# Performance work log

Measured on AMD Instinct MI355X. Metric: run time of the kernel, lower is better.

## Reference

```python
import jax, jax.numpy as jnp
import numpy as np

D_MODEL = 1024
NUM_HEADS = 16
D_K = D_MODEL // NUM_HEADS
ROPE_BASE = 10000.0


def _rope_cos_sin(seq_len, d_k):
    inv_freq = 1.0 / (ROPE_BASE ** (jnp.arange(0, d_k, 2, dtype=jnp.float32) / d_k))
    t = jnp.arange(seq_len, dtype=jnp.float32)
    freqs = t[:, None] * inv_freq[None, :]          # [S, d_k/2]
    emb = jnp.concatenate([freqs, freqs], axis=-1)  # [S, d_k]
    return jnp.cos(emb), jnp.sin(emb)


def _rotate_half(x):
    x1, x2 = jnp.split(x, 2, axis=-1)
    return jnp.concatenate([-x2, x1], axis=-1)


def setup_inputs() -> dict:
    key = jax.random.key(0)
    ks = jax.random.split(key, 11)
    B, S, D = 4, 2048, D_MODEL
    scale = 1.0 / np.sqrt(D)
    inp = {
        "query": jax.random.normal(ks[0], (B, S, D), jnp.float32),
        "key": jax.random.normal(ks[1], (B, S, D), jnp.float32),
        "value": jax.random.normal(ks[2], (B, S, D), jnp.float32),
        "W_q": jax.random.normal(ks[3], (D, D), jnp.float32) * scale,
        "b_q": jnp.zeros((D,), jnp.float32),
        "W_k": jax.random.normal(ks[4], (D, D), jnp.float32) * scale,
        "b_k": jnp.zeros((D,), jnp.float32),
        "W_v": jax.random.normal(ks[5], (D, D), jnp.float32) * scale,
        "b_v": jnp.zeros((D,), jnp.float32),
        "W_o": jax.random.normal(ks[6], (D, D), jnp.float32) * scale,
        "b_o": jnp.zeros((D,), jnp.float32),
    }
    return inp


def reference(query, key, value, W_q, b_q, W_k, b_k, W_v, b_v, W_o, b_o):
    B, Sq, D = query.shape
    Sk = key.shape[1]
    H, dk = NUM_HEADS, D_K

    # QKV projections -> [B, H, S, dk]
    Q = (query @ W_q.T + b_q).reshape(B, Sq, H, dk).transpose(0, 2, 1, 3)
    K = (key @ W_k.T + b_k).reshape(B, Sk, H, dk).transpose(0, 2, 1, 3)
    V = (value @ W_v.T + b_v).reshape(B, Sk, H, dk).transpose(0, 2, 1, 3)

    # RoPE
    cos, sin = _rope_cos_sin(Sq, dk)  # [S, dk]
    cos = cos[None, None]
    sin = sin[None, None]
    Q = Q * cos + _rotate_half(Q) * sin
    K = K * cos + _rotate_half(K) * sin

    scores = jnp.einsum("bhqd,bhkd->bhqk", Q, K) / np.sqrt(dk)
    causal_mask = jnp.triu(jnp.ones((Sq, Sk), bool), k=1)
    scores = jnp.where(causal_mask[None, None], -jnp.inf, scores)
    attn = jax.nn.softmax(scores, axis=-1)
    context = jnp.einsum("bhqk,bhkd->bhqd", attn, V)
    context = context.transpose(0, 2, 1, 3).reshape(B, Sq, D)
    return context @ W_o.T + b_o
```

## Files before the change

kernel.cpp:

```cpp
#include <hip/hip_runtime.h>
#include <hip/hip_bf16.h>
#include <cstdint>
#include <cstddef>


typedef __attribute__((ext_vector_type(8))) short short8;
typedef __attribute__((ext_vector_type(4))) float f32x4;
typedef unsigned short u16;

#define SCALE_Q 0.18033688011112042f

__device__ __forceinline__ u16 f2bf(float f) {
  __hip_bfloat16 h = __float2bfloat16(f);
  return *reinterpret_cast<u16*>(&h);
}
__device__ __forceinline__ float bf2f(short bits) {
  unsigned int u = ((unsigned int)(u16)bits) << 16;
  return __uint_as_float(u);
}
__device__ __forceinline__ void gload_lds16(const void* g, void* l) {
  __builtin_amdgcn_global_load_lds(
      (const __attribute__((address_space(1))) void*)g,
      (__attribute__((address_space(3))) void*)l, 16, 0, 0);
}
__device__ __forceinline__ f32x4 max4(f32x4 a, f32x4 b) {
  f32x4 r;
  r[0] = fmaxf(a[0], b[0]); r[1] = fmaxf(a[1], b[1]);
  r[2] = fmaxf(a[2], b[2]); r[3] = fmaxf(a[3], b[3]);
  return r;
}

struct CvtJobs {
  const float* src[7];
  u16* dst[7];
  int pref[8];
};

__global__ void cvt_all(CvtJobs jobs, int total4) {
  const int stride = gridDim.x * blockDim.x;
  for (int i = blockIdx.x * blockDim.x + threadIdx.x; i < total4; i += stride) {
    int j = 0;
#pragma unroll
    for (int t = 1; t < 7; ++t) j += (i >= jobs.pref[t]);
    const int off = i - jobs.pref[j];
    const float4 v = ((const float4*)jobs.src[j])[off];
    ushort4 o;
    o.x = f2bf(v.x); o.y = f2bf(v.y); o.z = f2bf(v.z); o.w = f2bf(v.w);
    ((ushort4*)jobs.dst[j])[off] = o;
  }
}

__global__ void rope_tables(float* __restrict__ cost, float* __restrict__ sint, int S) {
  const int idx = blockIdx.x * blockDim.x + threadIdx.x;
  if (idx >= S * 32) return;
  const int s = idx >> 5, i = idx & 31;
  const float invf = powf(10000.0f, -(float)i * (1.0f / 32.0f));
  const float ang = (float)s * invf;
  cost[idx] = cosf(ang);
  sint[idx] = sinf(ang);
}

template<int MODE>
__global__ __launch_bounds__(256, 2)
void gemm_fused(const u16* __restrict__ A, const u16* __restrict__ Bt,
                const float* __restrict__ bias, void* __restrict__ Cout,
                const float* __restrict__ cost, const float* __restrict__ sint,
                int M, int N, int K, int S) {
  __shared__ u16 As[128 * 64];
  __shared__ u16 Bs[128 * 64];
  const int tid = threadIdx.x;
  const int wid = tid >> 6;
  const int lane = tid & 63;
  const int g = lane >> 4, c = lane & 15;

  const int xcd = blockIdx.x & 7;
  const int slot = blockIdx.x >> 3;
  const int mPerX = (M >> 7) >> 3;
  const int m0 = (xcd * mPerX + (slot % mPerX)) << 7;
  const int n0 = (slot / mPerX) << 7;

  const int wr = wid >> 1, wc = wid & 1;

  f32x4 acc[4][4];
#pragma unroll
  for (int i = 0; i < 4; ++i)
#pragma unroll
    for (int j = 0; j < 4; ++j) acc[i][j] = (f32x4)(0.0f);

  const int kIters = K >> 6;
  for (int kt = 0; kt < kIters; ++kt) {
    const int k0 = kt << 6;
#pragma unroll
    for (int i = 0; i < 4; ++i) {
      const int chunk = i * 256 + tid;
      const int row = chunk >> 3;
      const int scz = (chunk & 7) ^ (row & 7);
      gload_lds16(A + (size_t)(m0 + row) * K + (k0 + scz * 8),
                  (char*)As + (size_t)(i * 256 + (wid << 6)) * 16);
      gload_lds16(Bt + (size_t)(n0 + row) * K + (k0 + scz * 8),
                  (char*)Bs + (size_t)(i * 256 + (wid << 6)) * 16);
    }
    __syncthreads();
#pragma unroll
    for (int ks = 0; ks < 2; ++ks) {
      short8 af[4], bfr[4];
#pragma unroll
      for (int mi = 0; mi < 4; ++mi) {
        const int row = wr * 64 + mi * 16 + c;
        const int cch = (g + ks * 4) ^ (row & 7);
        af[mi] = *(const short8*)((const char*)As + row * 128 + cch * 16);
      }
#pragma unroll
      for (int ni = 0; ni < 4; ++ni) {
        const int row = wc * 64 + ni * 16 + c;
        const int cch = (g + ks * 4) ^ (row & 7);
        bfr[ni] = *(const short8*)((const char*)Bs + row * 128 + cch * 16);
      }
#pragma unroll
      for (int mi = 0; mi < 4; ++mi)
#pragma unroll
        for (int ni = 0; ni < 4; ++ni)
          acc[mi][ni] = __builtin_amdgcn_mfma_f32_16x16x32_bf16(af[mi], bfr[ni], acc[mi][ni], 0, 0, 0);
    }
    __syncthreads();
  }

  float bv[4];
#pragma unroll
  for (int ni = 0; ni < 4; ++ni) bv[ni] = bias[n0 + wc * 64 + ni * 16 + c];

  if (MODE == 3) {
#pragma unroll
    for (int mi = 0; mi < 4; ++mi)
#pragma unroll
      for (int ni = 0; ni < 4; ++ni)
#pragma unroll
        for (int r = 0; r < 4; ++r) {
          const int row = m0 + wr * 64 + mi * 16 + g * 4 + r;
          const int col = n0 + wc * 64 + ni * 16 + c;
          ((float*)Cout)[(size_t)row * N + col] = acc[mi][ni][r] + bv[ni];
        }
  } else if (MODE == 2) {
#pragma unroll
    for (int mi = 0; mi < 4; ++mi) {
      const int row_base = m0 + wr * 64 + mi * 16 + g * 4;
      const int s = row_base & 2047;
      const int b = row_base >> 11;
#pragma unroll
      for (int ni = 0; ni < 4; ++ni) {
        const int col = n0 + wc * 64 + ni * 16 + c;
        const int h = col >> 6;
        const int d = ni * 16 + c;
        ushort4 w;
        w.x = f2bf(acc[mi][ni][0] + bv[ni]);
        w.y = f2bf(acc[mi][ni][1] + bv[ni]);
        w.z = f2bf(acc[mi][ni][2] + bv[ni]);
        w.w = f2bf(acc[mi][ni][3] + bv[ni]);
        *(ushort4*)((u16*)Cout + ((size_t)(b * 16 + h) * 64 + d) * (size_t)S + s) = w;
      }
    }
  } else {
#pragma unroll
    for (int mi = 0; mi < 4; ++mi)
#pragma unroll
      for (int pair = 0; pair < 2; ++pair) {
        const int d_lo = pair * 16 + c;
        const int col_lo = n0 + wc * 64 + d_lo;
        const int h = col_lo >> 6;
#pragma unroll
        for (int r = 0; r < 4; ++r) {
          const int row = m0 + wr * 64 + mi * 16 + g * 4 + r;
          const int s = row & 2047;
          const int b = row >> 11;
          const float co = cost[s * 32 + d_lo];
          const float si = sint[s * 32 + d_lo];
          const float vlo = acc[mi][pair][r] + bv[pair];
          const float vhi = acc[mi][pair + 2][r] + bv[pair + 2];
          float olo = vlo * co - vhi * si;
          float ohi = vhi * co + vlo * si;
          if (MODE == 0) { olo *= SCALE_Q; ohi *= SCALE_Q; }
          u16* dst = (u16*)Cout + ((size_t)(b * 16 + h) * S + s) * 64 + d_lo;
          dst[0]  = f2bf(olo);
          dst[32] = f2bf(ohi);
        }
      }
  }
}

__global__ __launch_bounds__(256, 4)
void attn_kernel(const u16* __restrict__ Qh, const u16* __restrict__ Kh,
                 const u16* __restrict__ Vt, u16* __restrict__ ctx,
                 int B, int H, int S) {
  __shared__ u16 KV[2][2][64 * 64];
  __shared__ u16 Ps[4][16 * 64];
  const int tid = threadIdx.x, wid = tid >> 6, lane = tid & 63;
  const int g = lane >> 4, c = lane & 15;

  const int id = blockIdx.x;
  const int j = id >> 8;
  const int x = id & 255;
  const int bh = x & 63;
  const int a = x >> 6;
  const int base = a + ((j >> 1) << 2);
  const int stile = (j & 1) ? (15 - base) : base;

  const int b = bh >> 4, h = bh & 15;
  const int D = H * 64;

  const size_t baseQK = (size_t)bh * S * 64;
  const size_t baseV  = (size_t)bh * 64 * S;

  const int q0 = stile * 128;
  const int KT = 2 * stile + 2;
  const int q0w = q0 + wid * 32;
  const int ktl = (q0w + 31) >> 6;
  const int qg0 = q0w + c, qg1 = q0w + 16 + c;

  short8 qB[2][2];
#pragma unroll
  for (int qf = 0; qf < 2; ++qf)
#pragma unroll
    for (int ks = 0; ks < 2; ++ks)
      qB[qf][ks] = *(const short8*)(Qh + baseQK +
                     (size_t)(q0w + qf * 16 + c) * 64 + ks * 32 + g * 8);

  float m_r[2], l_r[2];
  m_r[0] = m_r[1] = -__builtin_inff();
  l_r[0] = l_r[1] = 0.0f;
  f32x4 o[4][2];
#pragma unroll
  for (int df = 0; df < 4; ++df) { o[df][0] = (f32x4)(0.0f); o[df][1] = (f32x4)(0.0f); }

  auto stage = [&](int buf, int kt) {
#pragma unroll
    for (int i = 0; i < 2; ++i) {
      const int chunk = i * 256 + tid;
      const int row = chunk >> 3;
      const int scz = (chunk & 7) ^ (row & 7);
      gload_lds16(Kh + baseQK + (size_t)(kt * 64 + row) * 64 + scz * 8,
                  (char*)&KV[buf][0][0] + (size_t)(i * 256 + (wid << 6)) * 16);
      gload_lds16(Vt + baseV + (size_t)row * S + (kt * 64 + scz * 8),
                  (char*)&KV[buf][1][0] + (size_t)(i * 256 + (wid << 6)) * 16);
    }
  };

  stage(0, 0);
  __syncthreads();
  int cur = 0;
  for (int kt = 0; kt < KT; ++kt) {
    if (kt + 1 < KT) stage(cur ^ 1, kt + 1);
    if (kt <= ktl) {
      const char* Kb = (const char*)&KV[cur][0][0];
      const char* Vb = (const char*)&KV[cur][1][0];

      f32x4 sc[4][2];
#pragma unroll
      for (int kf = 0; kf < 4; ++kf) { sc[kf][0] = (f32x4)(0.0f); sc[kf][1] = (f32x4)(0.0f); }
      __builtin_amdgcn_s_setprio(1);
#pragma unroll
      for (int ks = 0; ks < 2; ++ks) {
        short8 kA[4];
#pragma unroll
        for (int kf = 0; kf < 4; ++kf) {
          const int row = kf * 16 + c;
          kA[kf] = *(const short8*)(Kb + row * 128 + (((g + 4 * ks) ^ (row & 7))) * 16);
        }
#pragma unroll
        for (int kf = 0; kf < 4; ++kf) {
          sc[kf][0] = __builtin_amdgcn_mfma_f32_16x16x32_bf16(kA[kf], qB[0][ks], sc[kf][0], 0, 0, 0);
          sc[kf][1] = __builtin_amdgcn_mfma_f32_16x16x32_bf16(kA[kf], qB[1][ks], sc[kf][1], 0, 0, 0);
        }
      }
      __builtin_amdgcn_s_setprio(0);

      if (kt == ktl) {
#pragma unroll
        for (int kf = 0; kf < 4; ++kf)
#pragma unroll
          for (int r = 0; r < 4; ++r) {
            const int kg = kt * 64 + kf * 16 + 4 * g + r;
            if (kg > qg0) sc[kf][0][r] = -__builtin_inff();
            if (kg > qg1) sc[kf][1][r] = -__builtin_inff();
          }
      }

      u16* Pw = &Ps[wid][0];
      short8 pB[2][2];
#pragma unroll
      for (int qf = 0; qf < 2; ++qf) {
        f32x4 mm = max4(max4(sc[0][qf], sc[1][qf]), max4(sc[2][qf], sc[3][qf]));
        float pm = fmaxf(fmaxf(mm[0], mm[1]), fmaxf(mm[2], mm[3]));
        pm = fmaxf(pm, __shfl_xor(pm, 16));
        pm = fmaxf(pm, __shfl_xor(pm, 32));
        if (__any(pm > m_r[qf] + 8.0f)) {
          const float mn = fmaxf(m_r[qf], pm);
          const float rs = __builtin_exp2f(m_r[qf] - mn);
          m_r[qf] = mn; l_r[qf] *= rs;
#pragma unroll
          for (int df = 0; df < 4; ++df) o[df][qf] *= rs;
        }
        f32x4 ps4 = (f32x4)(0.0f);
#pragma unroll
        for (int kf = 0; kf < 4; ++kf) {
          f32x4 pv;
#pragma unroll
          for (int r = 0; r < 4; ++r) pv[r] = __builtin_exp2f(sc[kf][qf][r] - m_r[qf]);
          sc[kf][qf] = pv;
          ps4 += pv;
        }
        float psum = (ps4[0] + ps4[1]) + (ps4[2] + ps4[3]);
        psum += __shfl_xor(psum, 16);
        psum += __shfl_xor(psum, 32);
        l_r[qf] += psum;

#pragma unroll
        for (int kf = 0; kf < 4; ++kf) {
          ushort4 pk;
          pk.x = f2bf(sc[kf][qf][0]); pk.y = f2bf(sc[kf][qf][1]);
          pk.z = f2bf(sc[kf][qf][2]); pk.w = f2bf(sc[kf][qf][3]);
          *(ushort4*)((char*)Pw + c * 128 +
                      (((2 * kf + (g >> 1)) ^ (c & 7))) * 16 + 8 * (g & 1)) = pk;
        }
#pragma unroll
        for (int ks = 0; ks < 2; ++ks)
          pB[qf][ks] = *(const short8*)((const char*)Pw + c * 128 +
                                        (((g + 4 * ks) ^ (c & 7))) * 16);
      }

      __builtin_amdgcn_s_setprio(1);
#pragma unroll
      for (int ks = 0; ks < 2; ++ks)
#pragma unroll
        for (int df = 0; df < 4; ++df) {
          const int row = df * 16 + c;
          const short8 va = *(const short8*)(Vb + row * 128 + (((g + 4 * ks) ^ (row & 7))) * 16);
          o[df][0] = __builtin_amdgcn_mfma_f32_16x16x32_bf16(va, pB[0][ks], o[df][0], 0, 0, 0);
          o[df][1] = __builtin_amdgcn_mfma_f32_16x16x32_bf16(va, pB[1][ks], o[df][1], 0, 0, 0);
        }
      __builtin_amdgcn_s_setprio(0);
    }
    __syncthreads();
    cur ^= 1;
  }

#pragma unroll
  for (int qf = 0; qf < 2; ++qf) {
    const float inv = 1.0f / l_r[qf];
    u16* rowp = ctx + (size_t)(b * S + q0w + qf * 16 + c) * D + h * 64;
#pragma unroll
    for (int df = 0; df < 4; ++df) {
      ushort4 w;
      w.x = f2bf(o[df][qf][0] * inv); w.y = f2bf(o[df][qf][1] * inv);
      w.z = f2bf(o[df][qf][2] * inv); w.w = f2bf(o[df][qf][3] * inv);
      *(ushort4*)(rowp + df * 16 + 4 * g) = w;
    }
  }
}

extern "C" void kernel_launch(void* const* d_in, const int* in_sizes, int n_in,
                              void* d_out, int out_size, void* d_ws, size_t ws_size,
                              hipStream_t stream) {
  const float* query = (const float*)d_in[0];
  const float* key   = (const float*)d_in[1];
  const float* value = (const float*)d_in[2];
  const float* W_q = (const float*)d_in[3];
  const float* b_q = (const float*)d_in[4];
  const float* W_k = (const float*)d_in[5];
  const float* b_k = (const float*)d_in[6];
  const float* W_v = (const float*)d_in[7];
  const float* b_v = (const float*)d_in[8];
  const float* W_o = (const float*)d_in[9];
  const float* b_o = (const float*)d_in[10];

  const int D = 1024, H = 16, S = 2048;
  const int BS = in_sizes[0] / D;
  const int B = BS / S;

  const size_t nX = (size_t)BS * D;
  const size_t nW = (size_t)D * D;
  u16* p = (u16*)d_ws;
  u16* xq = p;  p += nX;
  u16* xk = p;  p += nX;
  u16* xv = p;  p += nX;
  u16* wq = p;  p += nW;
  u16* wk = p;  p += nW;
  u16* wv = p;  p += nW;
  u16* wo = p;  p += nW;
  u16* Qh = p;  p += nX;
  u16* Kh = p;  p += nX;
  u16* Vtr = p; p += nX;
  float* cost = (float*)p;
  float* sint = cost + (size_t)S * 32;
  u16* ctx = xq;

  CvtJobs jobs;
  jobs.src[0] = query; jobs.src[1] = key; jobs.src[2] = value;
  jobs.src[3] = W_q;   jobs.src[4] = W_k; jobs.src[5] = W_v; jobs.src[6] = W_o;
  jobs.dst[0] = xq; jobs.dst[1] = xk; jobs.dst[2] = xv;
  jobs.dst[3] = wq; jobs.dst[4] = wk; jobs.dst[5] = wv; jobs.dst[6] = wo;
  const int a4 = (int)(nX / 4), w4 = (int)(nW / 4);
  jobs.pref[0] = 0;
  jobs.pref[1] = a4;     jobs.pref[2] = 2 * a4; jobs.pref[3] = 3 * a4;
  jobs.pref[4] = 3 * a4 + w4;     jobs.pref[5] = 3 * a4 + 2 * w4;
  jobs.pref[6] = 3 * a4 + 3 * w4; jobs.pref[7] = 3 * a4 + 4 * w4;
  cvt_all<<<2048, 256, 0, stream>>>(jobs, jobs.pref[7]);

  rope_tables<<<(S * 32 + 255) / 256, 256, 0, stream>>>(cost, sint, S);

  const int gblocks = (BS / 128) * (D / 128);
  gemm_fused<0><<<gblocks, 256, 0, stream>>>(xq, wq, b_q, Qh,  cost, sint, BS, D, D, S);
  gemm_fused<1><<<gblocks, 256, 0, stream>>>(xk, wk, b_k, Kh,  cost, sint, BS, D, D, S);
  gemm_fused<2><<<gblocks, 256, 0, stream>>>(xv, wv, b_v, Vtr, cost, sint, BS, D, D, S);

  attn_kernel<<<(S / 128) * B * H, 256, 0, stream>>>(Qh, Kh, Vtr, ctx, B, H, S);

  gemm_fused<3><<<gblocks, 256, 0, stream>>>(ctx, wo, b_o, d_out, cost, sint, BS, D, D, S);
}
```

Baseline: 339.8 us.

## Fuse fp32-to-bf16 activation conversion into QKV GEMM loads; simplify attention tile order

The QKV projection GEMMs now read fp32 query/key/value directly, converting to bf16 in registers and writing the swizzled LDS tile. This drops the separate conversion pass over the three activation tensors and their bf16 copies. The cost is that the A operand no longer uses async global-to-LDS loads, and each tile reads twice the global bytes. The attention grid mapping also changes to a plain heaviest-tile-first order.

After: 402.5 us. +18.4%, slower.

```diff
diff --git a/kernel.cpp b/kernel.cpp
--- a/kernel.cpp
+++ b/kernel.cpp
@@ -60,14 +60,16 @@
   sint[idx] = sinf(ang);
 }
 
-template<int MODE>
+template<int MODE, int AF32>
 __global__ __launch_bounds__(256, 2)
-void gemm_fused(const u16* __restrict__ A, const u16* __restrict__ Bt,
+void gemm_fused(const void* __restrict__ Ain, const u16* __restrict__ Bt,
                 const float* __restrict__ bias, void* __restrict__ Cout,
                 const float* __restrict__ cost, const float* __restrict__ sint,
                 int M, int N, int K, int S) {
   __shared__ u16 As[128 * 64];
   __shared__ u16 Bs[128 * 64];
+  const u16* A16 = (const u16*)Ain;
+  const float* A32 = (const float*)Ain;
   const int tid = threadIdx.x;
   const int wid = tid >> 6;
   const int lane = tid & 63;
@@ -95,10 +97,35 @@
       const int chunk = i * 256 + tid;
       const int row = chunk >> 3;
       const int scz = (chunk & 7) ^ (row & 7);
-      gload_lds16(A + (size_t)(m0 + row) * K + (k0 + scz * 8),
-                  (char*)As + (size_t)(i * 256 + (wid << 6)) * 16);
       gload_lds16(Bt + (size_t)(n0 + row) * K + (k0 + scz * 8),
                   (char*)Bs + (size_t)(i * 256 + (wid << 6)) * 16);
+    }
+    if (AF32) {
+#pragma unroll
+      for (int i = 0; i < 4; ++i) {
+        const int chunk = i * 256 + tid;
+        const int row = chunk >> 3;
+        const int c8 = (chunk & 7) * 8;
+        const float* src = A32 + (size_t)(m0 + row) * K + k0 + c8;
+        const float4 f0 = *(const float4*)(src);
+        const float4 f1 = *(const float4*)(src + 4);
+        short8 v;
+        v[0] = (short)f2bf(f0.x); v[1] = (short)f2bf(f0.y);
+        v[2] = (short)f2bf(f0.z); v[3] = (short)f2bf(f0.w);
+        v[4] = (short)f2bf(f1.x); v[5] = (short)f2bf(f1.y);
+        v[6] = (short)f2bf(f1.z); v[7] = (short)f2bf(f1.w);
+        const int dst = (chunk & 7) ^ (row & 7);
+        *(short8*)((char*)As + row * 128 + dst * 16) = v;
+      }
+    } else {
+#pragma unroll
+      for (int i = 0; i < 4; ++i) {
+        const int chunk = i * 256 + tid;
+        const int row = chunk >> 3;
+        const int scz = (chunk & 7) ^ (row & 7);
+        gload_lds16(A16 + (size_t)(m0 + row) * K + (k0 + scz * 8),
+                    (char*)As + (size_t)(i * 256 + (wid << 6)) * 16);
+      }
     }
     __syncthreads();
 #pragma unroll
@@ -197,12 +224,8 @@
   const int g = lane >> 4, c = lane & 15;
 
   const int id = blockIdx.x;
-  const int j = id >> 8;
-  const int x = id & 255;
-  const int bh = x & 63;
-  const int a = x >> 6;
-  const int base = a + ((j >> 1) << 2);
-  const int stile = (j & 1) ? (15 - base) : base;
+  const int stile = 15 - (id >> 6);
+  const int bh = id & 63;
 
   const int b = bh >> 4, h = bh & 15;
   const int D = H * 64;
@@ -379,9 +402,7 @@
   const size_t nX = (size_t)BS * D;
   const size_t nW = (size_t)D * D;
   u16* p = (u16*)d_ws;
-  u16* xq = p;  p += nX;
-  u16* xk = p;  p += nX;
-  u16* xv = p;  p += nX;
+  u16* ctx = p; p += nX;
   u16* wq = p;  p += nW;
   u16* wk = p;  p += nW;
   u16* wv = p;  p += nW;
@@ -391,28 +412,26 @@
   u16* Vtr = p; p += nX;
   float* cost = (float*)p;
   float* sint = cost + (size_t)S * 32;
-  u16* ctx = xq;
 
   CvtJobs jobs;
-  jobs.src[0] = query; jobs.src[1] = key; jobs.src[2] = value;
-  jobs.src[3] = W_q;   jobs.src[4] = W_k; jobs.src[5] = W_v; jobs.src[6] = W_o;
-  jobs.dst[0] = xq; jobs.dst[1] = xk; jobs.dst[2] = xv;
-  jobs.dst[3] = wq; jobs.dst[4] = wk; jobs.dst[5] = wv; jobs.dst[6] = wo;
-  const int a4 = (int)(nX / 4), w4 = (int)(nW / 4);
-  jobs.pref[0] = 0;
-  jobs.pref[1] = a4;     jobs.pref[2] = 2 * a4; jobs.pref[3] = 3 * a4;
-  jobs.pref[4] = 3 * a4 + w4;     jobs.pref[5] = 3 * a4 + 2 * w4;
-  jobs.pref[6] = 3 * a4 + 3 * w4; jobs.pref[7] = 3 * a4 + 4 * w4;
-  cvt_all<<<2048, 256, 0, stream>>>(jobs, jobs.pref[7]);
+  jobs.src[0] = W_q; jobs.src[1] = W_k; jobs.src[2] = W_v; jobs.src[3] = W_o;
+  jobs.src[4] = W_o; jobs.src[5] = W_o; jobs.src[6] = W_o;
+  jobs.dst[0] = wq; jobs.dst[1] = wk; jobs.dst[2] = wv; jobs.dst[3] = wo;
+  jobs.dst[4] = wo; jobs.dst[5] = wo; jobs.dst[6] = wo;
+  const int w4 = (int)(nW / 4);
+  jobs.pref[0] = 0; jobs.pref[1] = w4; jobs.pref[2] = 2 * w4;
+  jobs.pref[3] = 3 * w4; jobs.pref[4] = 4 * w4;
+  jobs.pref[5] = 4 * w4; jobs.pref[6] = 4 * w4; jobs.pref[7] = 4 * w4;
+  cvt_all<<<512, 256, 0, stream>>>(jobs, 4 * w4);
 
   rope_tables<<<(S * 32 + 255) / 256, 256, 0, stream>>>(cost, sint, S);
 
   const int gblocks = (BS / 128) * (D / 128);
-  gemm_fused<0><<<gblocks, 256, 0, stream>>>(xq, wq, b_q, Qh,  cost, sint, BS, D, D, S);
-  gemm_fused<1><<<gblocks, 256, 0, stream>>>(xk, wk, b_k, Kh,  cost, sint, BS, D, D, S);
-  gemm_fused<2><<<gblocks, 256, 0, stream>>>(xv, wv, b_v, Vtr, cost, sint, BS, D, D, S);
+  gemm_fused<0, 1><<<gblocks, 256, 0, stream>>>(query, wq, b_q, Qh,  cost, sint, BS, D, D, S);
+  gemm_fused<1, 1><<<gblocks, 256, 0, stream>>>(key,   wk, b_k, Kh,  cost, sint, BS, D, D, S);
+  gemm_fused<2, 1><<<gblocks, 256, 0, stream>>>(value, wv, b_v, Vtr, cost, sint, BS, D, D, S);
 
   attn_kernel<<<(S / 128) * B * H, 256, 0, stream>>>(Qh, Kh, Vtr, ctx, B, H, S);
 
-  gemm_fused<3><<<gblocks, 256, 0, stream>>>(ctx, wo, b_o, d_out, cost, sint, BS, D, D, S);
-}
+  gemm_fused<3, 0><<<gblocks, 256, 0, stream>>>(ctx, wo, b_o, d_out, cost, sint, BS, D, D, S);
+}
```

## Merge QKV GEMMs into one launch and simplify attention tile ordering

Applied to the files above, without the earlier changes.

Folds the three separate Q/K/V projection GEMM launches into a single kernel whose block index selects the mode, so more blocks run concurrently and fewer waves leave the GPU partly idle. It raises the launch-bounds occupancy hint from 2 to 3 blocks per CU for the GEMMs. The attention block mapping changes from a paired interleaved tile order to a simple longest-first causal order. Higher occupancy may increase register pressure or cause spills, and the new attention ordering changes load balance.

Result: faster. 323.3 us (-4.9%).

```diff
diff --git a/kernel.cpp b/kernel.cpp
--- a/kernel.cpp
+++ b/kernel.cpp
@@ -61,20 +61,18 @@
 }
 
 template<int MODE>
-__global__ __launch_bounds__(256, 2)
-void gemm_fused(const u16* __restrict__ A, const u16* __restrict__ Bt,
-                const float* __restrict__ bias, void* __restrict__ Cout,
-                const float* __restrict__ cost, const float* __restrict__ sint,
-                int M, int N, int K, int S) {
-  __shared__ u16 As[128 * 64];
-  __shared__ u16 Bs[128 * 64];
+__device__ __forceinline__
+void gemm_body(int bid, const u16* __restrict__ A, const u16* __restrict__ Bt,
+               const float* __restrict__ bias, void* __restrict__ Cout,
+               const float* __restrict__ cost, const float* __restrict__ sint,
+               int M, int N, int K, int S, u16* As, u16* Bs) {
   const int tid = threadIdx.x;
   const int wid = tid >> 6;
   const int lane = tid & 63;
   const int g = lane >> 4, c = lane & 15;
 
-  const int xcd = blockIdx.x & 7;
-  const int slot = blockIdx.x >> 3;
+  const int xcd = bid & 7;
+  const int slot = bid >> 3;
   const int mPerX = (M >> 7) >> 3;
   const int m0 = (xcd * mPerX + (slot % mPerX)) << 7;
   const int n0 = (slot / mPerX) << 7;
@@ -187,6 +185,37 @@
   }
 }
 
+__global__ __launch_bounds__(256, 3)
+void qkv_gemm(const u16* __restrict__ xq, const u16* __restrict__ xk,
+              const u16* __restrict__ xv,
+              const u16* __restrict__ wq, const u16* __restrict__ wk,
+              const u16* __restrict__ wv,
+              const float* __restrict__ bq, const float* __restrict__ bk,
+              const float* __restrict__ bv,
+              u16* __restrict__ Qh, u16* __restrict__ Kh, u16* __restrict__ Vtr,
+              const float* __restrict__ cost, const float* __restrict__ sint,
+              int M, int N, int K, int S) {
+  __shared__ u16 As[128 * 64];
+  __shared__ u16 Bs[128 * 64];
+  const int mode = blockIdx.x >> 9;
+  const int bid = blockIdx.x & 511;
+  if (mode == 0)
+    gemm_body<0>(bid, xq, wq, bq, Qh, cost, sint, M, N, K, S, As, Bs);
+  else if (mode == 1)
+    gemm_body<1>(bid, xk, wk, bk, Kh, cost, sint, M, N, K, S, As, Bs);
+  else
+    gemm_body<2>(bid, xv, wv, bv, Vtr, cost, sint, M, N, K, S, As, Bs);
+}
+
+__global__ __launch_bounds__(256, 3)
+void o_gemm(const u16* __restrict__ A, const u16* __restrict__ Bt,
+            const float* __restrict__ bias, float* __restrict__ Cout,
+            int M, int N, int K, int S) {
+  __shared__ u16 As[128 * 64];
+  __shared__ u16 Bs[128 * 64];
+  gemm_body<3>(blockIdx.x, A, Bt, bias, Cout, nullptr, nullptr, M, N, K, S, As, Bs);
+}
+
 __global__ __launch_bounds__(256, 4)
 void attn_kernel(const u16* __restrict__ Qh, const u16* __restrict__ Kh,
                  const u16* __restrict__ Vt, u16* __restrict__ ctx,
@@ -197,12 +226,8 @@
   const int g = lane >> 4, c = lane & 15;
 
   const int id = blockIdx.x;
-  const int j = id >> 8;
-  const int x = id & 255;
-  const int bh = x & 63;
-  const int a = x >> 6;
-  const int base = a + ((j >> 1) << 2);
-  const int stile = (j & 1) ? (15 - base) : base;
+  const int stile = 15 - (id >> 6);
+  const int bh = id & 63;
 
   const int b = bh >> 4, h = bh & 15;
   const int D = H * 64;
@@ -407,12 +432,11 @@
 
   rope_tables<<<(S * 32 + 255) / 256, 256, 0, stream>>>(cost, sint, S);
 
-  const int gblocks = (BS / 128) * (D / 128);
-  gemm_fused<0><<<gblocks, 256, 0, stream>>>(xq, wq, b_q, Qh,  cost, sint, BS, D, D, S);
-  gemm_fused<1><<<gblocks, 256, 0, stream>>>(xk, wk, b_k, Kh,  cost, sint, BS, D, D, S);
-  gemm_fused<2><<<gblocks, 256, 0, stream>>>(xv, wv, b_v, Vtr, cost, sint, BS, D, D, S);
+  qkv_gemm<<<3 * 512, 256, 0, stream>>>(xq, xk, xv, wq, wk, wv,
+                                        b_q, b_k, b_v, Qh, Kh, Vtr,
+                                        cost, sint, BS, D, D, S);
 
   attn_kernel<<<(S / 128) * B * H, 256, 0, stream>>>(Qh, Kh, Vtr, ctx, B, H, S);
 
-  gemm_fused<3><<<gblocks, 256, 0, stream>>>(ctx, wo, b_o, d_out, cost, sint, BS, D, D, S);
-}
+  o_gemm<<<512, 256, 0, stream>>>(ctx, wo, b_o, (float*)d_out, BS, D, D, S);
+}
```
